# Optimization experiments

Measured on AMD Instinct MI355X. Metric: run time of the kernel, lower is better.

Reference implementation:

```python
import jax, jax.numpy as jnp
import numpy as np

GROUP = 64  # quantization group size along the input dim


def dequantize(W_q, scale, zero):
    """int4 dequant: W_q uint8-packed [out, in/2] (two nibbles per byte),
    group-wise affine scale/zero [out, in/GROUP]. Returns float [out, in]."""
    out, half = W_q.shape
    hi = (W_q >> 4) & 0xF
    lo = W_q & 0xF
    w = jnp.stack([hi, lo], axis=-1).reshape(out, half * 2).astype(scale.dtype)
    w = w.reshape(out, -1, GROUP)  # [out, n_groups, GROUP]
    w = (w - zero[:, :, None]) * scale[:, :, None]
    return w.reshape(out, half * 2)


def setup_inputs() -> dict:
    key = jax.random.key(0)
    ks = jax.random.split(key, 10)
    hidden, inter = 4096, 11008
    B, S = 4, 1024
    x = jax.random.normal(ks[0], (B, S, hidden), dtype=jnp.float32)
    gate_Wq = jax.random.randint(ks[1], (inter, hidden // 2), 0, 256, dtype=jnp.int32)
    up_Wq = jax.random.randint(ks[2], (inter, hidden // 2), 0, 256, dtype=jnp.int32)
    down_Wq = jax.random.randint(ks[3], (hidden, inter // 2), 0, 256, dtype=jnp.int32)
    # small scales keep activations sane; zero points in [0, 15]
    gate_scale = jax.random.uniform(ks[4], (inter, hidden // GROUP)) * 0.01 + 1e-4
    gate_zero = jax.random.uniform(ks[5], (inter, hidden // GROUP)) * 15.0
    up_scale = jax.random.uniform(ks[6], (inter, hidden // GROUP)) * 0.01 + 1e-4
    up_zero = jax.random.uniform(ks[7], (inter, hidden // GROUP)) * 15.0
    down_scale = jax.random.uniform(ks[8], (hidden, inter // GROUP)) * 0.01 + 1e-4
    down_zero = jax.random.uniform(ks[9], (hidden, inter // GROUP)) * 15.0
    return {"x": x, "gate_Wq": gate_Wq, "up_Wq": up_Wq, "down_Wq": down_Wq,
            "gate_scale": gate_scale, "gate_zero": gate_zero,
            "up_scale": up_scale, "up_zero": up_zero,
            "down_scale": down_scale, "down_zero": down_zero}


def reference(x, gate_Wq, up_Wq, down_Wq, gate_scale, gate_zero,
              up_scale, up_zero, down_scale, down_zero):
    Wg = dequantize(gate_Wq, gate_scale, gate_zero)  # [inter, hidden]
    Wu = dequantize(up_Wq, up_scale, up_zero)        # [inter, hidden]
    Wd = dequantize(down_Wq, down_scale, down_zero)  # [hidden, inter]
    g = jnp.einsum('bsh,ih->bsi', x, Wg)
    u = jnp.einsum('bsh,ih->bsi', x, Wu)
    h = jax.nn.silu(g) * u
    return jnp.einsum('bsi,hi->bsh', h, Wd)
```

## Files before the change

kernel.cpp:

```cpp
#include <hip/hip_runtime.h>
#include <hip/hip_fp16.h>
#include <cstdint>
#include <cstddef>

#define HIDDEN 4096
#define INTER  11008
#define NTOK   4096
#define NG1    (HIDDEN/64)
#define NG2    (INTER/64)

typedef _Float16 f16;
typedef _Float16 f16x8 __attribute__((ext_vector_type(8)));
typedef float    f32x4 __attribute__((ext_vector_type(4)));

__device__ __forceinline__ void g2lds16(const void* g, void* l) {
  __builtin_amdgcn_global_load_lds(
      (const __attribute__((address_space(1))) uint32_t*)g,
      (__attribute__((address_space(3))) uint32_t*)l, 16, 0, 0);
}

__device__ __forceinline__ uint32_t dq2(uint32_t b, __half2 s2, __half2 nzs) {
  uint32_t qb = 0x64006400u | (b >> 4) | ((b & 0xFu) << 16);
  __half2 hq = __builtin_bit_cast(__half2, qb);
  __half2 t  = __hsub2(hq, __builtin_bit_cast(__half2, 0x64006400u));
  __half2 wv = __hfma2(t, s2, nzs);
  return __builtin_bit_cast(uint32_t, wv);
}

__global__ __launch_bounds__(256) void cvt_x(const float* __restrict__ x,
                                             f16* __restrict__ xh) {
  size_t i = ((size_t)blockIdx.x * 256 + threadIdx.x) * 8;
  float4 a = *(const float4*)(x + i);
  float4 b = *(const float4*)(x + i + 4);
  f16x8 o = {(f16)a.x, (f16)a.y, (f16)a.z, (f16)a.w,
             (f16)b.x, (f16)b.y, (f16)b.z, (f16)b.w};
  *(f16x8*)(xh + i) = o;
}

__global__ __launch_bounds__(512) void gemm_gateup(
    const f16* __restrict__ xh,
    const uint32_t* __restrict__ gq, const uint32_t* __restrict__ uq,
    const float* __restrict__ gs, const float* __restrict__ gz,
    const float* __restrict__ us, const float* __restrict__ uz,
    f16* __restrict__ h) {
  __shared__ f16 lA[256 * 64];
  __shared__ f16 lBg[64 * 64];
  __shared__ f16 lBu[64 * 64];
  const int tid = threadIdx.x, lane = tid & 63, wave = tid >> 6;
  const int bm = blockIdx.x, bn = blockIdx.y;
  const int wm = wave >> 1, wn = wave & 1;

  const int arow0 = tid >> 3;
  const int ak8s  = (tid & 7) ^ (arow0 & 7);
  const f16* aptr = xh + (size_t)(bm * 256 + arow0) * HIDDEN + ak8s * 8;
  char* aldst = (char*)lA + tid * 16;

  const int mat = tid >> 8;
  const int t = tid & 255;
  const int brow0 = t >> 3;
  const uint32_t* qp = (mat ? uq : gq) + (size_t)(bn * 64 + brow0) * (HIDDEN / 2) + (t & 7) * 4;
  const float* sp = (mat ? us : gs) + (size_t)(bn * 64 + brow0) * NG1;
  const float* zp = (mat ? uz : gz) + (size_t)(bn * 64 + brow0) * NG1;
  char* lb = (char*)(mat ? lBu : lBg);
  const int bws0 = brow0 * 128 + (((t & 7) ^ (brow0 & 7)) << 4);

  int abase[4], asel[4];
#pragma unroll
  for (int im = 0; im < 4; ++im) {
    int r = wm * 64 + im * 16 + (lane & 15);
    abase[im] = r * 128; asel[im] = r & 7;
  }
  int bbase[2], bsel[2];
#pragma unroll
  for (int in_ = 0; in_ < 2; ++in_) {
    int r = wn * 32 + in_ * 16 + (lane & 15);
    bbase[in_] = r * 128; bsel[in_] = r & 7;
  }
  const int kchunk = lane >> 4;

  f32x4 accg[4][2] = {};
  f32x4 accu[4][2] = {};

  for (int kt = 0; kt < NG1; ++kt) {
    __syncthreads();
#pragma unroll
    for (int i = 0; i < 4; ++i)
      g2lds16(aptr + (size_t)i * 64 * HIDDEN, aldst + i * 512 * 16);
    {
      uint4 w0 = *(const uint4*)qp;
      uint4 w1 = *(const uint4*)(qp + (size_t)32 * (HIDDEN / 2));
      float s0f = sp[kt], z0f = zp[kt];
      float s1f = sp[32 * NG1 + kt], z1f = zp[32 * NG1 + kt];
      __half2 s0 = __float2half2_rn(s0f), n0 = __float2half2_rn(-z0f * s0f);
      __half2 s1 = __float2half2_rn(s1f), n1 = __float2half2_rn(-z1f * s1f);
      uint4 o0, o1;
      o0.x = dq2(w0.x, s0, n0); o0.y = dq2(w0.y, s0, n0);
      o0.z = dq2(w0.z, s0, n0); o0.w = dq2(w0.w, s0, n0);
      o1.x = dq2(w1.x, s1, n1); o1.y = dq2(w1.y, s1, n1);
      o1.z = dq2(w1.z, s1, n1); o1.w = dq2(w1.w, s1, n1);
      *(uint4*)(lb + bws0) = o0;
      *(uint4*)(lb + bws0 + 32 * 128) = o1;
    }
    __syncthreads();
#pragma unroll
    for (int ks = 0; ks < 2; ++ks) {
      int kc = ks * 4 + kchunk;
      f16x8 a[4], bg[2], bu[2];
#pragma unroll
      for (int im = 0; im < 4; ++im)
        a[im] = *(const f16x8*)((const char*)lA + abase[im] + ((kc ^ asel[im]) << 4));
#pragma unroll
      for (int in_ = 0; in_ < 2; ++in_) {
        bg[in_] = *(const f16x8*)((const char*)lBg + bbase[in_] + ((kc ^ bsel[in_]) << 4));
        bu[in_] = *(const f16x8*)((const char*)lBu + bbase[in_] + ((kc ^ bsel[in_]) << 4));
      }
#pragma unroll
      for (int im = 0; im < 4; ++im)
#pragma unroll
        for (int in_ = 0; in_ < 2; ++in_) {
          accg[im][in_] = __builtin_amdgcn_mfma_f32_16x16x32_f16(a[im], bg[in_], accg[im][in_], 0, 0, 0);
          accu[im][in_] = __builtin_amdgcn_mfma_f32_16x16x32_f16(a[im], bu[in_], accu[im][in_], 0, 0, 0);
        }
    }
    aptr += 64;
    qp += 32;
  }
#pragma unroll
  for (int im = 0; im < 4; ++im)
#pragma unroll
    for (int in_ = 0; in_ < 2; ++in_)
#pragma unroll
      for (int r = 0; r < 4; ++r) {
        int row = bm * 256 + wm * 64 + im * 16 + (lane >> 4) * 4 + r;
        int col = bn * 64 + wn * 32 + in_ * 16 + (lane & 15);
        float g = accg[im][in_][r];
        float u = accu[im][in_][r];
        float hv = (g / (1.0f + __expf(-g))) * u;
        h[(size_t)row * INTER + col] = (f16)hv;
      }
}

__global__ __launch_bounds__(512) void gemm_down(
    const f16* __restrict__ h, const uint32_t* __restrict__ dq_,
    const float* __restrict__ dsc, const float* __restrict__ dz,
    float* __restrict__ out) {
  __shared__ f16 lA[256 * 64];
  __shared__ f16 lB[128 * 64];
  const int tid = threadIdx.x, lane = tid & 63, wave = tid >> 6;
  const int bm = blockIdx.x, bn = blockIdx.y;
  const int wm = wave >> 1, wn = wave & 1;

  const int arow0 = tid >> 3;
  const int ak8s  = (tid & 7) ^ (arow0 & 7);
  const f16* aptr = h + (size_t)(bm * 256 + arow0) * INTER + ak8s * 8;
  char* aldst = (char*)lA + tid * 16;

  const int brow0 = tid >> 3;
  const uint32_t* qp = dq_ + (size_t)(bn * 128 + brow0) * (INTER / 2) + (tid & 7) * 4;
  const float* sp = dsc + (size_t)(bn * 128 + brow0) * NG2;
  const float* zp = dz + (size_t)(bn * 128 + brow0) * NG2;
  const int bws0 = brow0 * 128 + (((tid & 7) ^ (brow0 & 7)) << 4);

  int abase[4], asel[4];
#pragma unroll
  for (int im = 0; im < 4; ++im) {
    int r = wm * 64 + im * 16 + (lane & 15);
    abase[im] = r * 128; asel[im] = r & 7;
  }
  int bbase[4], bsel[4];
#pragma unroll
  for (int in_ = 0; in_ < 4; ++in_) {
    int r = wn * 64 + in_ * 16 + (lane & 15);
    bbase[in_] = r * 128; bsel[in_] = r & 7;
  }
  const int kchunk = lane >> 4;

  f32x4 acc[4][4] = {};

  for (int kt = 0; kt < NG2; ++kt) {
    __syncthreads();
#pragma unroll
    for (int i = 0; i < 4; ++i)
      g2lds16(aptr + (size_t)i * 64 * INTER, aldst + i * 512 * 16);
    {
      uint4 w0 = *(const uint4*)qp;
      uint4 w1 = *(const uint4*)(qp + (size_t)64 * (INTER / 2));
      float s0f = sp[kt], z0f = zp[kt];
      float s1f = sp[64 * NG2 + kt], z1f = zp[64 * NG2 + kt];
      __half2 s0 = __float2half2_rn(s0f), n0 = __float2half2_rn(-z0f * s0f);
      __half2 s1 = __float2half2_rn(s1f), n1 = __float2half2_rn(-z1f * s1f);
      uint4 o0, o1;
      o0.x = dq2(w0.x, s0, n0); o0.y = dq2(w0.y, s0, n0);
      o0.z = dq2(w0.z, s0, n0); o0.w = dq2(w0.w, s0, n0);
      o1.x = dq2(w1.x, s1, n1); o1.y = dq2(w1.y, s1, n1);
      o1.z = dq2(w1.z, s1, n1); o1.w = dq2(w1.w, s1, n1);
      *(uint4*)((char*)lB + bws0) = o0;
      *(uint4*)((char*)lB + bws0 + 64 * 128) = o1;
    }
    __syncthreads();
#pragma unroll
    for (int ks = 0; ks < 2; ++ks) {
      int kc = ks * 4 + kchunk;
      f16x8 a[4], b[4];
#pragma unroll
      for (int im = 0; im < 4; ++im)
        a[im] = *(const f16x8*)((const char*)lA + abase[im] + ((kc ^ asel[im]) << 4));
#pragma unroll
      for (int in_ = 0; in_ < 4; ++in_)
        b[in_] = *(const f16x8*)((const char*)lB + bbase[in_] + ((kc ^ bsel[in_]) << 4));
#pragma unroll
      for (int im = 0; im < 4; ++im)
#pragma unroll
        for (int in_ = 0; in_ < 4; ++in_)
          acc[im][in_] = __builtin_amdgcn_mfma_f32_16x16x32_f16(a[im], b[in_], acc[im][in_], 0, 0, 0);
    }
    aptr += 64;
    qp += 32;
  }
#pragma unroll
  for (int im = 0; im < 4; ++im)
#pragma unroll
    for (int in_ = 0; in_ < 4; ++in_)
#pragma unroll
      for (int r = 0; r < 4; ++r) {
        int row = bm * 256 + wm * 64 + im * 16 + (lane >> 4) * 4 + r;
        int col = bn * 128 + wn * 64 + in_ * 16 + (lane & 15);
        out[(size_t)row * HIDDEN + col] = acc[im][in_][r];
      }
}

extern "C" void kernel_launch(void* const* d_in, const int* in_sizes, int n_in,
                              void* d_out, int out_size, void* d_ws, size_t ws_size,
                              hipStream_t stream) {
  const float*    x   = (const float*)d_in[0];
  const uint32_t* gq  = (const uint32_t*)d_in[1];
  const uint32_t* uq  = (const uint32_t*)d_in[2];
  const uint32_t* dqw = (const uint32_t*)d_in[3];
  const float*    gs  = (const float*)d_in[4];
  const float*    gz  = (const float*)d_in[5];
  const float*    us  = (const float*)d_in[6];
  const float*    uz  = (const float*)d_in[7];
  const float*    dsc = (const float*)d_in[8];
  const float*    dzz = (const float*)d_in[9];

  f16* xh   = (f16*)d_ws;
  f16* hbuf = (f16*)((char*)d_ws + (size_t)NTOK * HIDDEN * 2);
  float* out = (float*)d_out;

  cvt_x<<<dim3((NTOK * HIDDEN) / (256 * 8)), 256, 0, stream>>>(x, xh);
  gemm_gateup<<<dim3(NTOK / 256, INTER / 64), 512, 0, stream>>>(
      xh, gq, uq, gs, gz, us, uz, hbuf);
  gemm_down<<<dim3(NTOK / 256, HIDDEN / 128), 512, 0, stream>>>(
      hbuf, dqw, dsc, dzz, out);
}
```

Baseline: 1.548 ms.

## Double-buffer activation tiles and prefetch quantized weights across K iterations

```diff
diff --git a/kernel.cpp b/kernel.cpp
--- a/kernel.cpp
+++ b/kernel.cpp
@@ -37,15 +37,17 @@
   *(f16x8*)(xh + i) = o;
 }
 
-__global__ __launch_bounds__(512) void gemm_gateup(
+__global__ __launch_bounds__(512, 4) void gemm_gateup(
     const f16* __restrict__ xh,
     const uint32_t* __restrict__ gq, const uint32_t* __restrict__ uq,
     const float* __restrict__ gs, const float* __restrict__ gz,
     const float* __restrict__ us, const float* __restrict__ uz,
     f16* __restrict__ h) {
-  __shared__ f16 lA[256 * 64];
-  __shared__ f16 lBg[64 * 64];
-  __shared__ f16 lBu[64 * 64];
+  extern __shared__ char smem[];
+  f16* lA0 = (f16*)smem;
+  f16* lA1 = (f16*)(smem + 32768);
+  char* lBg = smem + 65536;
+  char* lBu = smem + 73728;
   const int tid = threadIdx.x, lane = tid & 63, wave = tid >> 6;
   const int bm = blockIdx.x, bn = blockIdx.y;
   const int wm = wave >> 1, wn = wave & 1;
@@ -53,7 +55,7 @@
   const int arow0 = tid >> 3;
   const int ak8s  = (tid & 7) ^ (arow0 & 7);
   const f16* aptr = xh + (size_t)(bm * 256 + arow0) * HIDDEN + ak8s * 8;
-  char* aldst = (char*)lA + tid * 16;
+  const int aoff = tid * 16;
 
   const int mat = tid >> 8;
   const int t = tid & 255;
@@ -61,7 +63,7 @@
   const uint32_t* qp = (mat ? uq : gq) + (size_t)(bn * 64 + brow0) * (HIDDEN / 2) + (t & 7) * 4;
   const float* sp = (mat ? us : gs) + (size_t)(bn * 64 + brow0) * NG1;
   const float* zp = (mat ? uz : gz) + (size_t)(bn * 64 + brow0) * NG1;
-  char* lb = (char*)(mat ? lBu : lBg);
+  char* lb = mat ? lBu : lBg;
   const int bws0 = brow0 * 128 + (((t & 7) ^ (brow0 & 7)) << 4);
 
   int abase[4], asel[4];
@@ -81,27 +83,30 @@
   f32x4 accg[4][2] = {};
   f32x4 accu[4][2] = {};
 
-  for (int kt = 0; kt < NG1; ++kt) {
-    __syncthreads();
+  auto stageA = [&](const f16* src, f16* dst) {
 #pragma unroll
     for (int i = 0; i < 4; ++i)
-      g2lds16(aptr + (size_t)i * 64 * HIDDEN, aldst + i * 512 * 16);
-    {
-      uint4 w0 = *(const uint4*)qp;
-      uint4 w1 = *(const uint4*)(qp + (size_t)32 * (HIDDEN / 2));
-      float s0f = sp[kt], z0f = zp[kt];
-      float s1f = sp[32 * NG1 + kt], z1f = zp[32 * NG1 + kt];
-      __half2 s0 = __float2half2_rn(s0f), n0 = __float2half2_rn(-z0f * s0f);
-      __half2 s1 = __float2half2_rn(s1f), n1 = __float2half2_rn(-z1f * s1f);
-      uint4 o0, o1;
-      o0.x = dq2(w0.x, s0, n0); o0.y = dq2(w0.y, s0, n0);
-      o0.z = dq2(w0.z, s0, n0); o0.w = dq2(w0.w, s0, n0);
-      o1.x = dq2(w1.x, s1, n1); o1.y = dq2(w1.y, s1, n1);
-      o1.z = dq2(w1.z, s1, n1); o1.w = dq2(w1.w, s1, n1);
-      *(uint4*)(lb + bws0) = o0;
-      *(uint4*)(lb + bws0 + 32 * 128) = o1;
-    }
-    __syncthreads();
+      g2lds16(src + (size_t)i * 64 * HIDDEN, (char*)dst + aoff + i * 8192);
+  };
+  auto loadB = [&](int ktn, uint4& w0, uint4& w1,
+                   float& s0f, float& z0f, float& s1f, float& z1f) {
+    w0 = *(const uint4*)(qp + (size_t)ktn * 32);
+    w1 = *(const uint4*)(qp + (size_t)32 * (HIDDEN / 2) + (size_t)ktn * 32);
+    s0f = sp[ktn]; z0f = zp[ktn];
+    s1f = sp[32 * NG1 + ktn]; z1f = zp[32 * NG1 + ktn];
+  };
+  auto writeB = [&](uint4 w0, uint4 w1, float s0f, float z0f, float s1f, float z1f) {
+    __half2 s0 = __float2half2_rn(s0f), n0 = __float2half2_rn(-z0f * s0f);
+    __half2 s1 = __float2half2_rn(s1f), n1 = __float2half2_rn(-z1f * s1f);
+    uint4 o0, o1;
+    o0.x = dq2(w0.x, s0, n0); o0.y = dq2(w0.y, s0, n0);
+    o0.z = dq2(w0.z, s0, n0); o0.w = dq2(w0.w, s0, n0);
+    o1.x = dq2(w1.x, s1, n1); o1.y = dq2(w1.y, s1, n1);
+    o1.z = dq2(w1.z, s1, n1); o1.w = dq2(w1.w, s1, n1);
+    *(uint4*)(lb + bws0) = o0;
+    *(uint4*)(lb + bws0 + 32 * 128) = o1;
+  };
+  auto compute = [&](const f16* lA) {
 #pragma unroll
     for (int ks = 0; ks < 2; ++ks) {
       int kc = ks * 4 + kchunk;
@@ -111,8 +116,8 @@
         a[im] = *(const f16x8*)((const char*)lA + abase[im] + ((kc ^ asel[im]) << 4));
 #pragma unroll
       for (int in_ = 0; in_ < 2; ++in_) {
-        bg[in_] = *(const f16x8*)((const char*)lBg + bbase[in_] + ((kc ^ bsel[in_]) << 4));
-        bu[in_] = *(const f16x8*)((const char*)lBu + bbase[in_] + ((kc ^ bsel[in_]) << 4));
+        bg[in_] = *(const f16x8*)(lBg + bbase[in_] + ((kc ^ bsel[in_]) << 4));
+        bu[in_] = *(const f16x8*)(lBu + bbase[in_] + ((kc ^ bsel[in_]) << 4));
       }
 #pragma unroll
       for (int im = 0; im < 4; ++im)
@@ -122,9 +127,27 @@
           accu[im][in_] = __builtin_amdgcn_mfma_f32_16x16x32_f16(a[im], bu[in_], accu[im][in_], 0, 0, 0);
         }
     }
-    aptr += 64;
-    qp += 32;
-  }
+  };
+
+  stageA(aptr, lA0);
+  {
+    uint4 w0, w1; float s0f, z0f, s1f, z1f;
+    loadB(0, w0, w1, s0f, z0f, s1f, z1f);
+    writeB(w0, w1, s0f, z0f, s1f, z1f);
+  }
+  __syncthreads();
+
+  for (int kt = 0; kt < NG1 - 1; ++kt) {
+    stageA(aptr + (size_t)(kt + 1) * 64, (kt & 1) ? lA0 : lA1);
+    uint4 w0, w1; float s0f, z0f, s1f, z1f;
+    loadB(kt + 1, w0, w1, s0f, z0f, s1f, z1f);
+    compute((kt & 1) ? lA1 : lA0);
+    __syncthreads();
+    writeB(w0, w1, s0f, z0f, s1f, z1f);
+    __syncthreads();
+  }
+  compute(((NG1 - 1) & 1) ? lA1 : lA0);
+
 #pragma unroll
   for (int im = 0; im < 4; ++im)
 #pragma unroll
@@ -140,12 +163,14 @@
       }
 }
 
-__global__ __launch_bounds__(512) void gemm_down(
+__global__ __launch_bounds__(512, 4) void gemm_down(
     const f16* __restrict__ h, const uint32_t* __restrict__ dq_,
     const float* __restrict__ dsc, const float* __restrict__ dz,
     float* __restrict__ out) {
-  __shared__ f16 lA[256 * 64];
-  __shared__ f16 lB[128 * 64];
+  extern __shared__ char smem[];
+  f16* lA0 = (f16*)smem;
+  f16* lA1 = (f16*)(smem + 32768);
+  char* lB = smem + 65536;
   const int tid = threadIdx.x, lane = tid & 63, wave = tid >> 6;
   const int bm = blockIdx.x, bn = blockIdx.y;
   const int wm = wave >> 1, wn = wave & 1;
@@ -153,7 +178,7 @@
   const int arow0 = tid >> 3;
   const int ak8s  = (tid & 7) ^ (arow0 & 7);
   const f16* aptr = h + (size_t)(bm * 256 + arow0) * INTER + ak8s * 8;
-  char* aldst = (char*)lA + tid * 16;
+  const int aoff = tid * 16;
 
   const int brow0 = tid >> 3;
   const uint32_t* qp = dq_ + (size_t)(bn * 128 + brow0) * (INTER / 2) + (tid & 7) * 4;
@@ -177,27 +202,30 @@
 
   f32x4 acc[4][4] = {};
 
-  for (int kt = 0; kt < NG2; ++kt) {
-    __syncthreads();
+  auto stageA = [&](const f16* src, f16* dst) {
 #pragma unroll
     for (int i = 0; i < 4; ++i)
-      g2lds16(aptr + (size_t)i * 64 * INTER, aldst + i * 512 * 16);
-    {
-      uint4 w0 = *(const uint4*)qp;
-      uint4 w1 = *(const uint4*)(qp + (size_t)64 * (INTER / 2));
-      float s0f = sp[kt], z0f = zp[kt];
-      float s1f = sp[64 * NG2 + kt], z1f = zp[64 * NG2 + kt];
-      __half2 s0 = __float2half2_rn(s0f), n0 = __float2half2_rn(-z0f * s0f);
-      __half2 s1 = __float2half2_rn(s1f), n1 = __float2half2_rn(-z1f * s1f);
-      uint4 o0, o1;
-      o0.x = dq2(w0.x, s0, n0); o0.y = dq2(w0.y, s0, n0);
-      o0.z = dq2(w0.z, s0, n0); o0.w = dq2(w0.w, s0, n0);
-      o1.x = dq2(w1.x, s1, n1); o1.y = dq2(w1.y, s1, n1);
-      o1.z = dq2(w1.z, s1, n1); o1.w = dq2(w1.w, s1, n1);
-      *(uint4*)((char*)lB + bws0) = o0;
-      *(uint4*)((char*)lB + bws0 + 64 * 128) = o1;
-    }
-    __syncthreads();
+      g2lds16(src + (size_t)i * 64 * INTER, (char*)dst + aoff + i * 8192);
+  };
+  auto loadB = [&](int ktn, uint4& w0, uint4& w1,
+                   float& s0f, float& z0f, float& s1f, float& z1f) {
+    w0 = *(const uint4*)(qp + (size_t)ktn * 32);
+    w1 = *(const uint4*)(qp + (size_t)64 * (INTER / 2) + (size_t)ktn * 32);
+    s0f = sp[ktn]; z0f = zp[ktn];
+    s1f = sp[64 * NG2 + ktn]; z1f = zp[64 * NG2 + ktn];
+  };
+  auto writeB = [&](uint4 w0, uint4 w1, float s0f, float z0f, float s1f, float z1f) {
+    __half2 s0 = __float2half2_rn(s0f), n0 = __float2half2_rn(-z0f * s0f);
+    __half2 s1 = __float2half2_rn(s1f), n1 = __float2half2_rn(-z1f * s1f);
+    uint4 o0, o1;
+    o0.x = dq2(w0.x, s0, n0); o0.y = dq2(w0.y, s0, n0);
+    o0.z = dq2(w0.z, s0, n0); o0.w = dq2(w0.w, s0, n0);
+    o1.x = dq2(w1.x, s1, n1); o1.y = dq2(w1.y, s1, n1);
+    o1.z = dq2(w1.z, s1, n1); o1.w = dq2(w1.w, s1, n1);
+    *(uint4*)(lB + bws0) = o0;
+    *(uint4*)(lB + bws0 + 64 * 128) = o1;
+  };
+  auto compute = [&](const f16* lA) {
 #pragma unroll
     for (int ks = 0; ks < 2; ++ks) {
       int kc = ks * 4 + kchunk;
@@ -207,16 +235,34 @@
         a[im] = *(const f16x8*)((const char*)lA + abase[im] + ((kc ^ asel[im]) << 4));
 #pragma unroll
       for (int in_ = 0; in_ < 4; ++in_)
-        b[in_] = *(const f16x8*)((const char*)lB + bbase[in_] + ((kc ^ bsel[in_]) << 4));
+        b[in_] = *(const f16x8*)(lB + bbase[in_] + ((kc ^ bsel[in_]) << 4));
 #pragma unroll
       for (int im = 0; im < 4; ++im)
 #pragma unroll
         for (int in_ = 0; in_ < 4; ++in_)
           acc[im][in_] = __builtin_amdgcn_mfma_f32_16x16x32_f16(a[im], b[in_], acc[im][in_], 0, 0, 0);
     }
-    aptr += 64;
-    qp += 32;
-  }
+  };
+
+  stageA(aptr, lA0);
+  {
+    uint4 w0, w1; float s0f, z0f, s1f, z1f;
+    loadB(0, w0, w1, s0f, z0f, s1f, z1f);
+    writeB(w0, w1, s0f, z0f, s1f, z1f);
+  }
+  __syncthreads();
+
+  for (int kt = 0; kt < NG2 - 1; ++kt) {
+    stageA(aptr + (size_t)(kt + 1) * 64, (kt & 1) ? lA0 : lA1);
+    uint4 w0, w1; float s0f, z0f, s1f, z1f;
+    loadB(kt + 1, w0, w1, s0f, z0f, s1f, z1f);
+    compute((kt & 1) ? lA1 : lA0);
+    __syncthreads();
+    writeB(w0, w1, s0f, z0f, s1f, z1f);
+    __syncthreads();
+  }
+  compute(((NG2 - 1) & 1) ? lA1 : lA0);
+
 #pragma unroll
   for (int im = 0; im < 4; ++im)
 #pragma unroll
@@ -247,9 +293,15 @@
   f16* hbuf = (f16*)((char*)d_ws + (size_t)NTOK * HIDDEN * 2);
   float* out = (float*)d_out;
 
+  const int LDS_BYTES = 80 * 1024;
+  (void)hipFuncSetAttribute((const void*)gemm_gateup,
+                            hipFuncAttributeMaxDynamicSharedMemorySize, LDS_BYTES);
+  (void)hipFuncSetAttribute((const void*)gemm_down,
+                            hipFuncAttributeMaxDynamicSharedMemorySize, LDS_BYTES);
+
   cvt_x<<<dim3((NTOK * HIDDEN) / (256 * 8)), 256, 0, stream>>>(x, xh);
-  gemm_gateup<<<dim3(NTOK / 256, INTER / 64), 512, 0, stream>>>(
+  gemm_gateup<<<dim3(NTOK / 256, INTER / 64), 512, LDS_BYTES, stream>>>(
       xh, gq, uq, gs, gz, us, uz, hbuf);
-  gemm_down<<<dim3(NTOK / 256, HIDDEN / 128), 512, 0, stream>>>(
+  gemm_down<<<dim3(NTOK / 256, HIDDEN / 128), 512, LDS_BYTES, stream>>>(
       hbuf, dqw, dsc, dzz, out);
 }
```

Result: no change. 1.519 ms (-1.9%).
